# Performance work log

Measured on AMD Instinct MI355X. Metric: run time of the kernel, lower is better.

Reference implementation:

```python
import jax, jax.numpy as jnp
import numpy as np

HIDDEN = 2048
N_HEAD = 16
N_KV_HEAD = 4
HEAD_DIM = HIDDEN // N_HEAD
B, S = 2, 2048


def setup_inputs() -> dict:
    key = jax.random.key(0)
    ks = jax.random.split(key, 10)
    scale = 1.0 / np.sqrt(HIDDEN)
    x = jax.random.normal(ks[0], (B, S, HIDDEN), dtype=jnp.float32)
    # causal additive mask, broadcastable over batch and heads
    causal = jnp.tril(jnp.ones((S, S), dtype=jnp.bool_))
    attention_mask = jnp.where(causal, 0.0, -1e9).astype(jnp.float32)[None, None]
    wq_w = jax.random.uniform(ks[1], (HIDDEN, HIDDEN), jnp.float32, -scale, scale)
    wq_b = jax.random.uniform(ks[2], (HIDDEN,), jnp.float32, -scale, scale)
    wk_w = jax.random.uniform(ks[3], (N_KV_HEAD * HEAD_DIM, HIDDEN), jnp.float32, -scale, scale)
    wk_b = jax.random.uniform(ks[4], (N_KV_HEAD * HEAD_DIM,), jnp.float32, -scale, scale)
    wv_w = jax.random.uniform(ks[5], (N_KV_HEAD * HEAD_DIM, HIDDEN), jnp.float32, -scale, scale)
    wv_b = jax.random.uniform(ks[6], (N_KV_HEAD * HEAD_DIM,), jnp.float32, -scale, scale)
    wo_w = jax.random.uniform(ks[7], (HIDDEN, HIDDEN), jnp.float32, -scale, scale)
    wo_b = jax.random.uniform(ks[8], (HIDDEN,), jnp.float32, -scale, scale)
    return dict(x=x, attention_mask=attention_mask, wq_w=wq_w, wq_b=wq_b,
                wk_w=wk_w, wk_b=wk_b, wv_w=wv_w, wv_b=wv_b, wo_w=wo_w, wo_b=wo_b)


def reference(x, attention_mask, wq_w, wq_b, wk_w, wk_b, wv_w, wv_b, wo_w, wo_b):
    bs, seq_len, _ = x.shape
    group = N_HEAD // N_KV_HEAD
    q = x @ wq_w.T + wq_b  # [B,S,H*D]
    k = x @ wk_w.T + wk_b  # [B,S,Hkv*D]
    v = x @ wv_w.T + wv_b
    q = q.reshape(bs, seq_len, N_HEAD, HEAD_DIM).transpose(0, 2, 1, 3)        # [B,H,S,D]
    k = k.reshape(bs, seq_len, N_KV_HEAD, HEAD_DIM).transpose(0, 2, 1, 3)     # [B,Hkv,S,D]
    v = v.reshape(bs, seq_len, N_KV_HEAD, HEAD_DIM).transpose(0, 2, 1, 3)
    # GQA: share each kv head across `group` query heads (repeat_interleave equiv)
    qg = q.reshape(bs, N_KV_HEAD, group, seq_len, HEAD_DIM)
    scores = jnp.einsum('bkgqd,bkld->bkgql', qg, k) / np.sqrt(HEAD_DIM)       # [B,Hkv,g,S,S]
    scores = scores + attention_mask[:, :, None]  # mask broadcast over head dims
    attn = jax.nn.softmax(scores, axis=-1)  # dropout is identity at inference
    out = jnp.einsum('bkgql,bkld->bkgqd', attn, v)                             # [B,Hkv,g,S,D]
    out = out.reshape(bs, N_HEAD, seq_len, HEAD_DIM).transpose(0, 2, 1, 3)
    out = out.reshape(bs, seq_len, HIDDEN)
    return out @ wo_w.T + wo_b
```

## Files before the change

kernel.cpp:

```cpp
#include <hip/hip_runtime.h>

typedef __bf16 bf16;
typedef __bf16 bf16x8 __attribute__((ext_vector_type(8)));
typedef __bf16 bf16x4 __attribute__((ext_vector_type(4)));
typedef __bf16 bf16x2 __attribute__((ext_vector_type(2)));
typedef float  f32x4  __attribute__((ext_vector_type(4)));

#define HIDDEN 2048
#define NH 16
#define NKV 4
#define HD 128
#define BB 2
#define SS 2048
#define MTOT (BB*SS)
#define KVD (NKV*HD)

__device__ __forceinline__ void gload_lds16(const void* g, void* l) {
  __builtin_amdgcn_global_load_lds(
      (__attribute__((address_space(1))) void*)(void*)g,
      (__attribute__((address_space(3))) void*)l,
      16, 0, 0);
}

__device__ __forceinline__ void pipe_barrier() {
  __builtin_amdgcn_sched_barrier(0);
  __builtin_amdgcn_s_barrier();
  __builtin_amdgcn_sched_barrier(0);
}

__global__ void detect_dtype(const unsigned short* __restrict__ x, int* __restrict__ flag) {
  __shared__ int cnt;
  if (threadIdx.x == 0) cnt = 0;
  __syncthreads();
  int c = 0;
  for (int i = threadIdx.x; i < 8192; i += blockDim.x) {
    float v = fabsf(__uint_as_float((unsigned)x[i] << 16));
    if (v > 64.0f || (v > 0.0f && v < 9.5367431640625e-07f)) ++c;
  }
  atomicAdd(&cnt, c);
  __syncthreads();
  if (threadIdx.x == 0) flag[0] = (cnt > 1024) ? 1 : 0;
}

struct ConvJobs {
  const void* src[8];
  bf16*       dst[8];
  long long   n[8];
};

__device__ __forceinline__ void conv8(const void* src, bf16* dst, long long n,
                                      int f, long long i0, long long stride) {
  const long long n8 = n >> 3;
  if (f) {
    const float4* s4 = (const float4*)src;
    for (long long i = i0; i < n8; i += stride) {
      float4 a = s4[2*i], b = s4[2*i+1];
      bf16x8 o;
      o[0]=(bf16)a.x; o[1]=(bf16)a.y; o[2]=(bf16)a.z; o[3]=(bf16)a.w;
      o[4]=(bf16)b.x; o[5]=(bf16)b.y; o[6]=(bf16)b.z; o[7]=(bf16)b.w;
      *(bf16x8*)&dst[i*8] = o;
    }
  } else {
    const bf16x8* s8 = (const bf16x8*)src;
    for (long long i = i0; i < n8; i += stride)
      *(bf16x8*)&dst[i*8] = s8[i];
  }
}

__global__ void conv_multi(ConvJobs jobs, const int* __restrict__ flag) {
  const int f = flag[0];
  const int a = blockIdx.y;
  conv8(jobs.src[a], jobs.dst[a], jobs.n[a], f,
        (long long)blockIdx.x * blockDim.x + threadIdx.x,
        (long long)gridDim.x * blockDim.x);
}

__global__ void conv_one(const void* __restrict__ src, bf16* __restrict__ dst,
                         long long n, const int* __restrict__ flag) {
  conv8(src, dst, n, flag[0],
        (long long)blockIdx.x * blockDim.x + threadIdx.x,
        (long long)gridDim.x * blockDim.x);
}

__global__ __launch_bounds__(512)
void gemm_qkv192(const bf16* __restrict__ A,
                 const bf16* __restrict__ wq, const bf16* __restrict__ bq,
                 const bf16* __restrict__ wk, const bf16* __restrict__ bk,
                 const bf16* __restrict__ wv, const bf16* __restrict__ bv,
                 bf16* __restrict__ Cq, bf16* __restrict__ Ck, bf16* __restrict__ Cvt)
{
  __shared__ bf16 Asl[2][256*32];
  __shared__ bf16 Bsl[2][192*32];
  const int bid = blockIdx.y * 16 + blockIdx.x;
  const int swz = (bid & 7) * 32 + (bid >> 3);
  const int bx  = swz & 15;
  const int by  = swz >> 4;

  const int tid  = threadIdx.x;
  const int wave = tid >> 6, lane = tid & 63;
  const int g = lane >> 4, l15 = lane & 15;
  const int wr = wave >> 2, wc = wave & 3;
  const int m0 = by * 256;
  const int n0 = bx * 192;

  f32x4 acc[8][3] = {};

  auto stage4 = [&](int nb, int k0) {
    #pragma unroll
    for (int li = 0; li < 4; ++li) {
      const int cid = tid + li * 512;
      if (cid < 1024) {
        const int row = cid >> 2, ch = cid & 3;
        const int sc  = ch ^ ((row >> 2) & 3);
        gload_lds16(A + (size_t)(m0 + row)*HIDDEN + k0 + sc*8, &Asl[nb][cid*8]);
      } else if (cid < 1792) {
        const int bcid = cid - 1024;
        const int row = bcid >> 2, ch = bcid & 3;
        const int sc  = ch ^ ((row >> 2) & 3);
        const int gc  = n0 + row;
        const bf16* wr2; int lr;
        if (gc < 2048)      { wr2 = wq; lr = gc; }
        else if (gc < 2560) { wr2 = wk; lr = gc - 2048; }
        else                { wr2 = wv; lr = gc - 2560; }
        gload_lds16(wr2 + (size_t)lr*HIDDEN + k0 + sc*8, &Bsl[nb][bcid*8]);
      }
    }
  };

  stage4(0, 0);
  asm volatile("s_waitcnt vmcnt(0)" ::: "memory");
  pipe_barrier();

  const int nt = HIDDEN / 32;
  int buf = 0;
  for (int t = 0; t < nt; ++t) {
    bf16x8 af[4], bfr[3];
    #pragma unroll
    for (int mi = 0; mi < 4; ++mi) {
      const int rl = wr*128 + mi*16 + l15;
      const int ch = g ^ ((rl >> 2) & 3);
      af[mi] = *(const bf16x8*)&Asl[buf][rl*32 + ch*8];
    }
    #pragma unroll
    for (int ni = 0; ni < 3; ++ni) {
      const int rl = wc*48 + ni*16 + l15;
      const int ch = g ^ ((rl >> 2) & 3);
      bfr[ni] = *(const bf16x8*)&Bsl[buf][rl*32 + ch*8];
    }
    if (t + 1 < nt) stage4(buf ^ 1, (t + 1) * 32);
    pipe_barrier();
    __builtin_amdgcn_s_setprio(1);
    #pragma unroll
    for (int mi = 0; mi < 4; ++mi)
      #pragma unroll
      for (int ni = 0; ni < 3; ++ni)
        acc[mi][ni] = __builtin_amdgcn_mfma_f32_16x16x32_bf16(af[mi], bfr[ni], acc[mi][ni], 0, 0, 0);
    __builtin_amdgcn_s_setprio(0);
    #pragma unroll
    for (int mi = 0; mi < 4; ++mi) {
      const int rl = wr*128 + 64 + mi*16 + l15;
      const int ch = g ^ ((rl >> 2) & 3);
      af[mi] = *(const bf16x8*)&Asl[buf][rl*32 + ch*8];
    }
    pipe_barrier();
    __builtin_amdgcn_s_setprio(1);
    #pragma unroll
    for (int mi = 0; mi < 4; ++mi)
      #pragma unroll
      for (int ni = 0; ni < 3; ++ni)
        acc[4+mi][ni] = __builtin_amdgcn_mfma_f32_16x16x32_bf16(af[mi], bfr[ni], acc[4+mi][ni], 0, 0, 0);
    __builtin_amdgcn_s_setprio(0);
    __builtin_amdgcn_sched_barrier(0);
    asm volatile("s_waitcnt vmcnt(0)" ::: "memory");
    __builtin_amdgcn_s_barrier();
    __builtin_amdgcn_sched_barrier(0);
    buf ^= 1;
  }

  #pragma unroll
  for (int ni = 0; ni < 3; ++ni) {
    const int gbase = n0 + wc*48 + ni*16;
    const int col   = gbase + l15;
    if (gbase < 2048) {
      const float bb = (float)bq[col];
      #pragma unroll
      for (int mi = 0; mi < 8; ++mi) {
        const int row = m0 + wr*128 + mi*16 + g*4;
        #pragma unroll
        for (int r = 0; r < 4; ++r)
          Cq[(size_t)(row + r)*HIDDEN + col] = (bf16)(acc[mi][ni][r] + bb);
      }
    } else if (gbase < 2560) {
      const int lc = col - 2048;
      const float bb = (float)bk[lc];
      #pragma unroll
      for (int mi = 0; mi < 8; ++mi) {
        const int row = m0 + wr*128 + mi*16 + g*4;
        #pragma unroll
        for (int r = 0; r < 4; ++r)
          Ck[(size_t)(row + r)*KVD + lc] = (bf16)(acc[mi][ni][r] + bb);
      }
    } else {
      const int cc = col - 2560;
      const float bb = (float)bv[cc];
      #pragma unroll
      for (int mi = 0; mi < 8; ++mi) {
        const int row = m0 + wr*128 + mi*16 + g*4;
        bf16x4 o4;
        #pragma unroll
        for (int r = 0; r < 4; ++r) o4[r] = (bf16)(acc[mi][ni][r] + bb);
        *(bf16x4*)&Cvt[(size_t)cc*MTOT + row] = o4;
      }
    }
  }
}

__global__ __launch_bounds__(256)
void gemm_bt(const bf16* __restrict__ A, const bf16* __restrict__ W,
             const bf16* __restrict__ bias, void* __restrict__ C,
             int M, int N, int K, const int* __restrict__ flagp)
{
  __shared__ bf16 As[128*32];
  __shared__ bf16 Bs[128*32];
  const int nwg = gridDim.x * gridDim.y;
  const int bid = blockIdx.y * gridDim.x + blockIdx.x;
  const int cpx = nwg >> 3;
  const int swz = (bid & 7) * cpx + (bid >> 3);
  const int bx  = swz % gridDim.x;
  const int by  = swz / gridDim.x;

  const int tid  = threadIdx.x;
  const int wave = tid >> 6, lane = tid & 63;
  const int g = lane >> 4, l15 = lane & 15;
  const int m0 = by * 128, n0 = bx * 128;
  const int wm = (wave >> 1) * 64, wn = (wave & 1) * 64;
  const int srow = lane >> 2;
  const int scol = (lane & 3) * 8;
  f32x4 acc[4][4] = {};

  for (int k0 = 0; k0 < K; k0 += 32) {
    #pragma unroll
    for (int i = 0; i < 2; ++i) {
      const int seg = wave*2 + i;
      const int row = seg*16 + srow;
      gload_lds16(A + (size_t)(m0+row)*K + k0 + scol, &As[row*32 + scol]);
      gload_lds16(W + (size_t)(n0+row)*K + k0 + scol, &Bs[row*32 + scol]);
    }
    asm volatile("s_waitcnt vmcnt(0)" ::: "memory");
    __syncthreads();
    bf16x8 af[4], bfr[4];
    #pragma unroll
    for (int m = 0; m < 4; ++m)
      af[m] = *(const bf16x8*)&As[(wm + m*16 + l15)*32 + g*8];
    #pragma unroll
    for (int n = 0; n < 4; ++n)
      bfr[n] = *(const bf16x8*)&Bs[(wn + n*16 + l15)*32 + g*8];
    #pragma unroll
    for (int m = 0; m < 4; ++m)
      #pragma unroll
      for (int n = 0; n < 4; ++n)
        acc[m][n] = __builtin_amdgcn_mfma_f32_16x16x32_bf16(af[m], bfr[n], acc[m][n], 0, 0, 0);
    __syncthreads();
  }
  const int outf = flagp ? flagp[0] : 0;
  if (outf) {
    float* Cf = (float*)C;
    #pragma unroll
    for (int n = 0; n < 4; ++n) {
      const int col = n0 + wn + n*16 + l15;
      const float bvv = (float)bias[col];
      #pragma unroll
      for (int m = 0; m < 4; ++m) {
        const int row = m0 + wm + m*16 + g*4;
        #pragma unroll
        for (int r = 0; r < 4; ++r)
          Cf[(size_t)(row + r)*N + col] = acc[m][n][r] + bvv;
      }
    }
  } else {
    bf16* Cb = (bf16*)C;
    #pragma unroll
    for (int n = 0; n < 4; ++n) {
      const int col = n0 + wn + n*16 + l15;
      const float bvv = (float)bias[col];
      #pragma unroll
      for (int m = 0; m < 4; ++m) {
        const int row = m0 + wm + m*16 + g*4;
        #pragma unroll
        for (int r = 0; r < 4; ++r)
          Cb[(size_t)(row + r)*N + col] = (bf16)(acc[m][n][r] + bvv);
      }
    }
  }
}

#define PPAD 72

__global__ __launch_bounds__(512)
void attn_fwd(const bf16* __restrict__ Q, const bf16* __restrict__ K,
              const bf16* __restrict__ Vt, bf16* __restrict__ O)
{
  __shared__ bf16 Ks[2][64*128];
  __shared__ bf16 Vs[128*64];
  __shared__ bf16 Pl[8][16][PPAD];
  const int tid = threadIdx.x, wave = tid >> 6, lane = tid & 63;
  const int g = lane >> 4, l15 = lane & 15;
  const int bh = blockIdx.y;
  const int b = bh >> 4, h = bh & 15, kvh = h >> 2;
  const bf16* Qh = Q + ((size_t)b*SS)*HIDDEN + h*HD;
  const bf16* Kh = K + ((size_t)b*SS)*KVD + kvh*HD;
  const bf16* Vh = Vt + ((size_t)kvh*HD)*MTOT + (size_t)b*SS;
  bf16*       Oh = O + ((size_t)b*SS)*HIDDEN + h*HD;

  const float KSC    = 0.12751879526563404f;
  const float NEGBIG = -1.0e30f;

  const int x      = blockIdx.x;
  const int qtB    = 31 - x;
  const int qtMine = (wave < 4) ? x : qtB;
  const int qrow0  = qtMine*64 + (wave & 3)*16;
  const int qg     = qrow0 + l15;

  bf16x8 bq[4];
  #pragma unroll
  for (int c = 0; c < 4; ++c)
    bq[c] = *(const bf16x8*)(Qh + (size_t)(qrow0 + l15)*HIDDEN + c*32 + g*8);

  f32x4 od[8] = {};
  float m_run = NEGBIG, l_part = 0.f;

  auto stageK = [&](int bi, int kv0) {
    #pragma unroll
    for (int i = 0; i < 2; ++i) {
      const int seg = wave*2 + i;
      const int kr  = seg*4 + (lane >> 4);
      const int kc  = (lane & 15) ^ (kr & 7);
      gload_lds16(Kh + (size_t)(kv0 + kr)*KVD + kc*8, &Ks[bi][seg*512 + lane*8]);
    }
  };
  auto stageV = [&](int kv0) {
    #pragma unroll
    for (int i = 0; i < 2; ++i) {
      const int seg = wave*2 + i;
      const int vr  = seg*8 + (lane >> 3);
      const int vc  = (lane & 7) ^ (lane >> 3);
      gload_lds16(Vh + (size_t)vr*MTOT + kv0 + vc*8, &Vs[seg*512 + lane*8]);
    }
  };

  stageK(0, 0);
  asm volatile("s_waitcnt vmcnt(0)" ::: "memory");
  __builtin_amdgcn_s_barrier();

  int buf = 0;
  #pragma unroll 1
  for (int t = 0; t <= qtB; ++t) {
    const int kv0 = t * 64;
    stageV(kv0);
    if (t < qtB) stageK(buf ^ 1, kv0 + 64);

    const bool active = (t <= qtMine);
    if (active) {
      f32x4 st[4];
      __builtin_amdgcn_s_setprio(1);
      #pragma unroll
      for (int nb = 0; nb < 4; ++nb) {
        f32x4 s = {};
        #pragma unroll
        for (int c = 0; c < 4; ++c) {
          const int krow = nb*16 + l15;
          const int kch  = (c*4 + g) ^ (krow & 7);
          bf16x8 ka = *(const bf16x8*)&Ks[buf][krow*128 + kch*8];
          s = __builtin_amdgcn_mfma_f32_16x16x32_bf16(ka, bq[c], s, 0, 0, 0);
        }
        st[nb] = s;
      }
      __builtin_amdgcn_s_setprio(0);

      float xx[16];
      float mt = NEGBIG;
      if (t == qtMine) {
        #pragma unroll
        for (int nb = 0; nb < 4; ++nb)
          #pragma unroll
          for (int r = 0; r < 4; ++r) {
            const int kv = kv0 + nb*16 + g*4 + r;
            float v = (kv <= qg) ? st[nb][r] : NEGBIG;
            xx[nb*4 + r] = v;
            mt = fmaxf(mt, v);
          }
      } else {
        #pragma unroll
        for (int nb = 0; nb < 4; ++nb)
          #pragma unroll
          for (int r = 0; r < 4; ++r) {
            xx[nb*4 + r] = st[nb][r];
            mt = fmaxf(mt, st[nb][r]);
          }
      }
      mt = fmaxf(mt, __shfl_xor(mt, 16, 64));
      mt = fmaxf(mt, __shfl_xor(mt, 32, 64));

      if (!__all((mt - m_run) <= 62.0f)) {
        const float m_new = fmaxf(m_run, mt);
        const float corr  = __builtin_amdgcn_exp2f((m_run - m_new) * KSC);
        l_part *= corr;
        #pragma unroll
        for (int db = 0; db < 8; ++db) od[db] *= corr;
        m_run = m_new;
      }

      float psum = 0.f;
      bf16x2 pk[4][2];
      #pragma unroll
      for (int nb = 0; nb < 4; ++nb) {
        const float p0 = __builtin_amdgcn_exp2f((xx[nb*4+0] - m_run) * KSC);
        const float p1 = __builtin_amdgcn_exp2f((xx[nb*4+1] - m_run) * KSC);
        const float p2 = __builtin_amdgcn_exp2f((xx[nb*4+2] - m_run) * KSC);
        const float p3 = __builtin_amdgcn_exp2f((xx[nb*4+3] - m_run) * KSC);
        psum += p0 + p1 + p2 + p3;
        pk[nb][0] = bf16x2{(bf16)p0, (bf16)p1};
        pk[nb][1] = bf16x2{(bf16)p2, (bf16)p3};
      }
      l_part += psum;

      #pragma unroll
      for (int nb = 0; nb < 4; ++nb) {
        *(bf16x2*)&Pl[wave][l15][nb*16 + g*4 + 0] = pk[nb][0];
        *(bf16x2*)&Pl[wave][l15][nb*16 + g*4 + 2] = pk[nb][1];
      }
    }

    if (t < qtB) { asm volatile("s_waitcnt vmcnt(2)" ::: "memory"); }
    else         { asm volatile("s_waitcnt vmcnt(0)" ::: "memory"); }
    __builtin_amdgcn_s_barrier();

    if (active) {
      asm volatile("s_waitcnt lgkmcnt(0)" ::: "memory");
      __builtin_amdgcn_sched_barrier(0);
      __builtin_amdgcn_s_setprio(1);
      #pragma unroll
      for (int c = 0; c < 2; ++c) {
        bf16x8 pb = *(const bf16x8*)&Pl[wave][l15][c*32 + g*8];
        #pragma unroll
        for (int db = 0; db < 8; ++db) {
          const int vrow = db*16 + l15;
          const int vch  = (c*4 + g) ^ (l15 & 7);
          bf16x8 va = *(const bf16x8*)&Vs[vrow*64 + vch*8];
          od[db] = __builtin_amdgcn_mfma_f32_16x16x32_bf16(va, pb, od[db], 0, 0, 0);
        }
      }
      __builtin_amdgcn_s_setprio(0);
    }

    asm volatile("s_waitcnt vmcnt(0)" ::: "memory");
    __builtin_amdgcn_s_barrier();
    buf ^= 1;
  }

  float lt = l_part;
  lt += __shfl_xor(lt, 16, 64);
  lt += __shfl_xor(lt, 32, 64);
  const float inv = 1.0f / lt;
  #pragma unroll
  for (int db = 0; db < 8; ++db) {
    bf16x4 o4;
    #pragma unroll
    for (int r = 0; r < 4; ++r) o4[r] = (bf16)(od[db][r] * inv);
    *(bf16x4*)(Oh + (size_t)qg*HIDDEN + db*16 + g*4) = o4;
  }
}

extern "C" void kernel_launch(void* const* d_in, const int* in_sizes, int n_in,
                              void* d_out, int out_size, void* d_ws, size_t ws_size,
                              hipStream_t stream)
{
  (void)in_sizes; (void)n_in; (void)out_size; (void)ws_size;
  const void* x    = d_in[0];
  const void* wq_w = d_in[2];
  const void* wq_b = d_in[3];
  const void* wk_w = d_in[4];
  const void* wk_b = d_in[5];
  const void* wv_w = d_in[6];
  const void* wv_b = d_in[7];
  const void* wo_w = d_in[8];
  const void* wo_b = d_in[9];

  int*  flag = (int*)d_ws;
  bf16* base = (bf16*)((char*)d_ws + 256);
  const long long NX  = (long long)MTOT*HIDDEN;
  const long long NWQ = (long long)HIDDEN*HIDDEN;
  const long long NWK = (long long)KVD*HIDDEN;
  bf16* x_ao = base;
  bf16* wqwo = x_ao + NX;
  bf16* wk_c = wqwo + NWQ;
  bf16* wv_c = wk_c + NWK;
  bf16* bq_c = wv_c + NWK;
  bf16* bk_c = bq_c + 2048;
  bf16* bv_c = bk_c + 512;
  bf16* bo_c = bv_c + 512;
  bf16* q_ws  = bo_c + 2048;
  bf16* k_ws  = q_ws + NX;
  bf16* vt_ws = k_ws + (long long)MTOT*KVD;

  detect_dtype<<<1, 256, 0, stream>>>((const unsigned short*)x, flag);

  ConvJobs jb;
  jb.src[0] = x;    jb.dst[0] = x_ao; jb.n[0] = NX;
  jb.src[1] = wq_w; jb.dst[1] = wqwo; jb.n[1] = NWQ;
  jb.src[2] = wk_w; jb.dst[2] = wk_c; jb.n[2] = NWK;
  jb.src[3] = wv_w; jb.dst[3] = wv_c; jb.n[3] = NWK;
  jb.src[4] = wq_b; jb.dst[4] = bq_c; jb.n[4] = 2048;
  jb.src[5] = wk_b; jb.dst[5] = bk_c; jb.n[5] = 512;
  jb.src[6] = wv_b; jb.dst[6] = bv_c; jb.n[6] = 512;
  jb.src[7] = wo_b; jb.dst[7] = bo_c; jb.n[7] = 2048;
  conv_multi<<<dim3(512, 8), 256, 0, stream>>>(jb, flag);

  gemm_qkv192<<<dim3(16, 16), 512, 0, stream>>>(x_ao, wqwo, bq_c, wk_c, bk_c,
                                                wv_c, bv_c, q_ws, k_ws, vt_ws);

  conv_one<<<dim3(512), 256, 0, stream>>>(wo_w, wqwo, NWQ, flag);

  attn_fwd<<<dim3(16, BB*NH), 512, 0, stream>>>(q_ws, k_ws, vt_ws, x_ao);

  gemm_bt<<<dim3(HIDDEN/128, MTOT/128), 256, 0, stream>>>(x_ao, wqwo, bo_c, d_out, MTOT, HIDDEN, HIDDEN, flag);
}
```

Baseline: 212.8 us.

## Double QKV GEMM K-tile to 64 and pass attention P via bpermute

The QKV projection GEMM now stages 64-wide K tiles (with an 8-way XOR swizzle) instead of 32, which halves the number of main-loop iterations and barriers at the cost of doubled LDS per buffer. In attention, the P tile is no longer written to and reread from shared memory; each lane gathers its P fragment from other lanes with ds_bpermute, which drops the Pl buffer and its lgkmcnt wait. The attention kernel also gains a min-blocks launch bound hint, which may push the compiler to limit registers and risk spills.

```diff
diff --git a/kernel.cpp b/kernel.cpp
--- a/kernel.cpp
+++ b/kernel.cpp
@@ -89,8 +89,8 @@
                  const bf16* __restrict__ wv, const bf16* __restrict__ bv,
                  bf16* __restrict__ Cq, bf16* __restrict__ Ck, bf16* __restrict__ Cvt)
 {
-  __shared__ bf16 Asl[2][256*32];
-  __shared__ bf16 Bsl[2][192*32];
+  __shared__ bf16 Asl[2][256*64];
+  __shared__ bf16 Bsl[2][192*64];
   const int bid = blockIdx.y * 16 + blockIdx.x;
   const int swz = (bid & 7) * 32 + (bid >> 3);
   const int bx  = swz & 15;
@@ -105,18 +105,18 @@
 
   f32x4 acc[8][3] = {};
 
-  auto stage4 = [&](int nb, int k0) {
-    #pragma unroll
-    for (int li = 0; li < 4; ++li) {
+  auto stage = [&](int nb, int k0) {
+    #pragma unroll
+    for (int li = 0; li < 7; ++li) {
       const int cid = tid + li * 512;
-      if (cid < 1024) {
-        const int row = cid >> 2, ch = cid & 3;
-        const int sc  = ch ^ ((row >> 2) & 3);
+      if (cid < 2048) {
+        const int row = cid >> 3, ch = cid & 7;
+        const int sc  = ch ^ (row & 7);
         gload_lds16(A + (size_t)(m0 + row)*HIDDEN + k0 + sc*8, &Asl[nb][cid*8]);
-      } else if (cid < 1792) {
-        const int bcid = cid - 1024;
-        const int row = bcid >> 2, ch = bcid & 3;
-        const int sc  = ch ^ ((row >> 2) & 3);
+      } else {
+        const int bcid = cid - 2048;
+        const int row = bcid >> 3, ch = bcid & 7;
+        const int sc  = ch ^ (row & 7);
         const int gc  = n0 + row;
         const bf16* wr2; int lr;
         if (gc < 2048)      { wr2 = wq; lr = gc; }
@@ -127,49 +127,52 @@
     }
   };
 
-  stage4(0, 0);
+  stage(0, 0);
   asm volatile("s_waitcnt vmcnt(0)" ::: "memory");
   pipe_barrier();
 
-  const int nt = HIDDEN / 32;
+  const int nt = HIDDEN / 64;
   int buf = 0;
   for (int t = 0; t < nt; ++t) {
     bf16x8 af[4], bfr[3];
     #pragma unroll
-    for (int mi = 0; mi < 4; ++mi) {
-      const int rl = wr*128 + mi*16 + l15;
-      const int ch = g ^ ((rl >> 2) & 3);
-      af[mi] = *(const bf16x8*)&Asl[buf][rl*32 + ch*8];
-    }
-    #pragma unroll
-    for (int ni = 0; ni < 3; ++ni) {
-      const int rl = wc*48 + ni*16 + l15;
-      const int ch = g ^ ((rl >> 2) & 3);
-      bfr[ni] = *(const bf16x8*)&Bsl[buf][rl*32 + ch*8];
-    }
-    if (t + 1 < nt) stage4(buf ^ 1, (t + 1) * 32);
-    pipe_barrier();
-    __builtin_amdgcn_s_setprio(1);
-    #pragma unroll
-    for (int mi = 0; mi < 4; ++mi)
-      #pragma unroll
-      for (int ni = 0; ni < 3; ++ni)
-        acc[mi][ni] = __builtin_amdgcn_mfma_f32_16x16x32_bf16(af[mi], bfr[ni], acc[mi][ni], 0, 0, 0);
-    __builtin_amdgcn_s_setprio(0);
-    #pragma unroll
-    for (int mi = 0; mi < 4; ++mi) {
-      const int rl = wr*128 + 64 + mi*16 + l15;
-      const int ch = g ^ ((rl >> 2) & 3);
-      af[mi] = *(const bf16x8*)&Asl[buf][rl*32 + ch*8];
-    }
-    pipe_barrier();
-    __builtin_amdgcn_s_setprio(1);
-    #pragma unroll
-    for (int mi = 0; mi < 4; ++mi)
-      #pragma unroll
-      for (int ni = 0; ni < 3; ++ni)
-        acc[4+mi][ni] = __builtin_amdgcn_mfma_f32_16x16x32_bf16(af[mi], bfr[ni], acc[4+mi][ni], 0, 0, 0);
-    __builtin_amdgcn_s_setprio(0);
+    for (int ks = 0; ks < 2; ++ks) {
+      #pragma unroll
+      for (int mi = 0; mi < 4; ++mi) {
+        const int rl = wr*128 + mi*16 + l15;
+        const int ch = (ks*4 + g) ^ (rl & 7);
+        af[mi] = *(const bf16x8*)&Asl[buf][rl*64 + ch*8];
+      }
+      #pragma unroll
+      for (int ni = 0; ni < 3; ++ni) {
+        const int rl = wc*48 + ni*16 + l15;
+        const int ch = (ks*4 + g) ^ (rl & 7);
+        bfr[ni] = *(const bf16x8*)&Bsl[buf][rl*64 + ch*8];
+      }
+      if (ks == 0 && t + 1 < nt) stage(buf ^ 1, (t + 1) * 64);
+      pipe_barrier();
+      __builtin_amdgcn_s_setprio(1);
+      #pragma unroll
+      for (int mi = 0; mi < 4; ++mi)
+        #pragma unroll
+        for (int ni = 0; ni < 3; ++ni)
+          acc[mi][ni] = __builtin_amdgcn_mfma_f32_16x16x32_bf16(af[mi], bfr[ni], acc[mi][ni], 0, 0, 0);
+      __builtin_amdgcn_s_setprio(0);
+      #pragma unroll
+      for (int mi = 0; mi < 4; ++mi) {
+        const int rl = wr*128 + 64 + mi*16 + l15;
+        const int ch = (ks*4 + g) ^ (rl & 7);
+        af[mi] = *(const bf16x8*)&Asl[buf][rl*64 + ch*8];
+      }
+      pipe_barrier();
+      __builtin_amdgcn_s_setprio(1);
+      #pragma unroll
+      for (int mi = 0; mi < 4; ++mi)
+        #pragma unroll
+        for (int ni = 0; ni < 3; ++ni)
+          acc[4+mi][ni] = __builtin_amdgcn_mfma_f32_16x16x32_bf16(af[mi], bfr[ni], acc[4+mi][ni], 0, 0, 0);
+      __builtin_amdgcn_s_setprio(0);
+    }
     __builtin_amdgcn_sched_barrier(0);
     asm volatile("s_waitcnt vmcnt(0)" ::: "memory");
     __builtin_amdgcn_s_barrier();
@@ -294,15 +297,12 @@
   }
 }
 
-#define PPAD 72
-
-__global__ __launch_bounds__(512)
+__global__ __launch_bounds__(512, 6)
 void attn_fwd(const bf16* __restrict__ Q, const bf16* __restrict__ K,
               const bf16* __restrict__ Vt, bf16* __restrict__ O)
 {
   __shared__ bf16 Ks[2][64*128];
   __shared__ bf16 Vs[128*64];
-  __shared__ bf16 Pl[8][16][PPAD];
   const int tid = threadIdx.x, wave = tid >> 6, lane = tid & 63;
   const int g = lane >> 4, l15 = lane & 15;
   const int bh = blockIdx.y;
@@ -329,6 +329,10 @@
   f32x4 od[8] = {};
   float m_run = NEGBIG, l_part = 0.f;
 
+  const int addrA = (((g & 1) * 2) * 16 + l15) * 4;
+  const int addrB = addrA + 64;
+  const bool hiG  = (g >> 1) != 0;
+
   auto stageK = [&](int bi, int kv0) {
     #pragma unroll
     for (int i = 0; i < 2; ++i) {
@@ -360,6 +364,7 @@
     if (t < qtB) stageK(buf ^ 1, kv0 + 64);
 
     const bool active = (t <= qtMine);
+    int ww[4][2];
     if (active) {
       f32x4 st[4];
       __builtin_amdgcn_s_setprio(1);
@@ -411,7 +416,6 @@
       }
 
       float psum = 0.f;
-      bf16x2 pk[4][2];
       #pragma unroll
       for (int nb = 0; nb < 4; ++nb) {
         const float p0 = __builtin_amdgcn_exp2f((xx[nb*4+0] - m_run) * KSC);
@@ -419,16 +423,12 @@
         const float p2 = __builtin_amdgcn_exp2f((xx[nb*4+2] - m_run) * KSC);
         const float p3 = __builtin_amdgcn_exp2f((xx[nb*4+3] - m_run) * KSC);
         psum += p0 + p1 + p2 + p3;
-        pk[nb][0] = bf16x2{(bf16)p0, (bf16)p1};
-        pk[nb][1] = bf16x2{(bf16)p2, (bf16)p3};
+        bf16x2 w0 = bf16x2{(bf16)p0, (bf16)p1};
+        bf16x2 w1 = bf16x2{(bf16)p2, (bf16)p3};
+        ww[nb][0] = *(int*)&w0;
+        ww[nb][1] = *(int*)&w1;
       }
       l_part += psum;
-
-      #pragma unroll
-      for (int nb = 0; nb < 4; ++nb) {
-        *(bf16x2*)&Pl[wave][l15][nb*16 + g*4 + 0] = pk[nb][0];
-        *(bf16x2*)&Pl[wave][l15][nb*16 + g*4 + 2] = pk[nb][1];
-      }
     }
 
     if (t < qtB) { asm volatile("s_waitcnt vmcnt(2)" ::: "memory"); }
@@ -436,12 +436,19 @@
     __builtin_amdgcn_s_barrier();
 
     if (active) {
-      asm volatile("s_waitcnt lgkmcnt(0)" ::: "memory");
-      __builtin_amdgcn_sched_barrier(0);
       __builtin_amdgcn_s_setprio(1);
       #pragma unroll
       for (int c = 0; c < 2; ++c) {
-        bf16x8 pb = *(const bf16x8*)&Pl[wave][l15][c*32 + g*8];
+        int wsel[4];
+        #pragma unroll
+        for (int j2 = 0; j2 < 4; ++j2) {
+          const int adr = (j2 >> 1) ? addrB : addrA;
+          const int a0 = __builtin_amdgcn_ds_bpermute(adr, ww[2*c + 0][j2 & 1]);
+          const int a1 = __builtin_amdgcn_ds_bpermute(adr, ww[2*c + 1][j2 & 1]);
+          wsel[j2] = hiG ? a1 : a0;
+        }
+        int4 pbi = {wsel[0], wsel[1], wsel[2], wsel[3]};
+        bf16x8 pb = *(bf16x8*)&pbi;
         #pragma unroll
         for (int db = 0; db < 8; ++db) {
           const int vrow = db*16 + l15;
```

Result: slower. 293.2 us (+37.8%).
